# Kernel tuning notes

Hardware: AMD Instinct MI355X
Metric: run time of the kernel (lower is better)

## Reference

```python
import jax, jax.numpy as jnp
import numpy as np

EPS = 1e-12  # torch F.normalize eps
NEG = -9999.0  # masked_fill value from the source


def _l2norm(x):
    n = jnp.linalg.norm(x, axis=-1, keepdims=True)
    return x / jnp.maximum(n, EPS)


def _maxsim(q, d, mask_f, mask_b):
    # q: [B,Lq,D]; d: [N,B,Ld,D]; mask: [N,B,Ld]
    rep = _l2norm(d * mask_f[..., None])
    s = jnp.einsum('bqd,nbkd->nbqk', q, rep)  # [N,B,Lq,Ld]
    s = jnp.where(mask_b[:, :, None, :], s, NEG)
    return s.max(axis=-1).sum(axis=-1)  # [N,B]


def setup_inputs() -> dict:
    key = jax.random.key(0)
    k0, k1, k2, k3, k4 = jax.random.split(key, 5)
    B, N, Lq, Ld, D = 128, 8, 32, 256, 128
    return {
        'q_reps': jax.random.normal(k0, (B, Lq, D), jnp.float32),
        'd_cq': jax.random.normal(k1, (N, B, Ld, D), jnp.float32),
        'd_orig': jax.random.normal(k2, (N, B, Ld, D), jnp.float32),
        'd_mask': jax.random.randint(k3, (N, B, Ld), 0, 2).astype(jnp.int32),
        'labels': jax.random.normal(k4, (B, N), jnp.float32),
    }


def reference(q_reps, d_cq, d_orig, d_mask, labels):
    # teacher='default', loss_type='kldiv' path
    q = _l2norm(q_reps)  # normalize query tokens over D
    mask_f = d_mask.astype(q_reps.dtype)
    mask_b = d_mask.astype(bool)
    scores = _maxsim(q, d_cq, mask_f, mask_b).T        # [B,N] student (cq) MaxSim
    scores_label = _maxsim(q, d_orig, mask_f, mask_b).T  # [B,N] teacher (orig) MaxSim
    # softmax->log in the source == log_softmax (same math, stable form)
    log_s = jax.nn.log_softmax(scores, axis=-1)
    log_t = jax.nn.log_softmax(scores_label, axis=-1)
    # KLDivLoss(reduction='batchmean', log_target=True)
    B = scores.shape[0]
    loss = jnp.sum(jnp.exp(log_t) * (log_t - log_s)) / B
    return loss
```

## Files before the change

### kernel.cpp

```cpp
#include <hip/hip_runtime.h>
#include <math.h>

#define Bq 128
#define Nn 8
#define LQ 32
#define LD 256
#define DD 128
#define EPSN 1e-12f
#define NEGV (-9999.0f)

typedef __attribute__((ext_vector_type(8))) short short8v;
typedef __attribute__((ext_vector_type(4))) int   int4v;
typedef __attribute__((ext_vector_type(4))) float f32x4;

__device__ __forceinline__ unsigned bf16_rne_hibits(float x) {
    unsigned u = __float_as_uint(x);
    return (u + 0x7FFFu + ((u >> 16) & 1u)) & 0xFFFF0000u;
}

__global__ __launch_bounds__(256) void qnorm_k(const float* __restrict__ q,
                                               unsigned short* __restrict__ qh,
                                               unsigned short* __restrict__ ql) {
    int row  = blockIdx.x * 4 + (threadIdx.x >> 6);
    int lane = threadIdx.x & 63;
    size_t base = (size_t)row * DD + lane * 2;
    float2 v = *reinterpret_cast<const float2*>(q + base);
    float ss = v.x * v.x + v.y * v.y;
#pragma unroll
    for (int o = 32; o; o >>= 1) ss += __shfl_xor(ss, o);
    float inv = 1.0f / fmaxf(sqrtf(ss), EPSN);
    float x0 = v.x * inv, x1 = v.y * inv;
    unsigned h0 = bf16_rne_hibits(x0), h1 = bf16_rne_hibits(x1);
    float l0 = x0 - __uint_as_float(h0);
    float l1 = x1 - __uint_as_float(h1);
    unsigned g0 = bf16_rne_hibits(l0), g1 = bf16_rne_hibits(l1);
    unsigned swz = ((unsigned)(lane * 2)) ^ (((unsigned)row & 7u) << 3);
    *reinterpret_cast<unsigned*>(qh + (size_t)row * DD + swz) = (h0 >> 16) | h1;
    *reinterpret_cast<unsigned*>(ql + (size_t)row * DD + swz) = (g0 >> 16) | g1;
}

__global__ __launch_bounds__(256) void maxsim_k(const float* __restrict__ d_cq,
                                                const float* __restrict__ d_orig,
                                                const int* __restrict__ mask,
                                                const unsigned short* __restrict__ qh,
                                                const unsigned short* __restrict__ ql,
                                                float* __restrict__ scores) {
    __shared__ float4 qstage[1024];
    __shared__ float wma[4][32];
    __shared__ float wmb[4][32];

    int nb = blockIdx.x;
    int b  = nb & 127;
    int n  = nb >> 7;

    int tid  = threadIdx.x;
    int w    = tid >> 6;
    int lane = tid & 63;
    int r    = lane & 15;
    int g    = lane >> 4;

    {
        const float4* srch = reinterpret_cast<const float4*>(qh + (size_t)b * LQ * DD);
        const float4* srcl = reinterpret_cast<const float4*>(ql + (size_t)b * LQ * DD);
        qstage[tid]       = srch[tid];
        qstage[tid + 256] = srch[tid + 256];
        qstage[tid + 512] = srcl[tid];
        qstage[tid + 768] = srcl[tid + 256];
    }
    __syncthreads();

    const unsigned short* qh_lds = reinterpret_cast<const unsigned short*>(qstage);
    const unsigned short* ql_lds = qh_lds + LQ * DD;
    unsigned swz8 = ((unsigned)r & 7u) << 3;

    f32x4 rm0a = {NEGV, NEGV, NEGV, NEGV}, rm1a = {NEGV, NEGV, NEGV, NEGV};
    f32x4 rm0b = {NEGV, NEGV, NEGV, NEGV}, rm1b = {NEGV, NEGV, NEGV, NEGV};

#define SB __builtin_amdgcn_sched_barrier(0)

#define CVT2(DH, DL, W, X0, X1, SSQ)                                           \
    { unsigned u0 = __float_as_uint(X0), u1 = __float_as_uint(X1);             \
      DH[W] = (int)((u0 >> 16) | (u1 & 0xFFFF0000u));                          \
      float l0 = (X0) - __uint_as_float(u0 & 0xFFFF0000u);                     \
      float l1 = (X1) - __uint_as_float(u1 & 0xFFFF0000u);                     \
      DL[W] = (int)((__float_as_uint(l0) >> 16) |                              \
                    (__float_as_uint(l1) & 0xFFFF0000u));                      \
      SSQ += (X0)*(X0) + (X1)*(X1); }

#define KSTEP(CA0, CA1, CB0, CB1, KS, PFOFF)                                   \
    {                                                                          \
        unsigned aoff = (((unsigned)(KS) * 32u) + (unsigned)g * 8u) ^ swz8;    \
        short8v a0h = *reinterpret_cast<const short8v*>(qh_lds + r * DD + aoff);          \
        short8v a0l = *reinterpret_cast<const short8v*>(ql_lds + r * DD + aoff);          \
        short8v a1h = *reinterpret_cast<const short8v*>(qh_lds + (r + 16) * DD + aoff);   \
        short8v a1l = *reinterpret_cast<const short8v*>(ql_lds + (r + 16) * DD + aoff);   \
        int4v dhwa, dlwa, dhwb, dlwb;                                          \
        CVT2(dhwa, dlwa, 0, CA0.x, CA0.y, ssqa)                                \
        CVT2(dhwa, dlwa, 1, CA0.z, CA0.w, ssqa)                                \
        CVT2(dhwa, dlwa, 2, CA1.x, CA1.y, ssqa)                                \
        CVT2(dhwa, dlwa, 3, CA1.z, CA1.w, ssqa)                                \
        CA0 = *reinterpret_cast<const float4*>(prow_a + (PFOFF));              \
        CA1 = *reinterpret_cast<const float4*>(prow_a + (PFOFF) + 4);          \
        CVT2(dhwb, dlwb, 0, CB0.x, CB0.y, ssqb)                                \
        CVT2(dhwb, dlwb, 1, CB0.z, CB0.w, ssqb)                                \
        CVT2(dhwb, dlwb, 2, CB1.x, CB1.y, ssqb)                                \
        CVT2(dhwb, dlwb, 3, CB1.z, CB1.w, ssqb)                                \
        CB0 = *reinterpret_cast<const float4*>(prow_b + (PFOFF));              \
        CB1 = *reinterpret_cast<const float4*>(prow_b + (PFOFF) + 4);          \
        short8v dha = __builtin_bit_cast(short8v, dhwa);                       \
        short8v dla = __builtin_bit_cast(short8v, dlwa);                       \
        c0a = __builtin_amdgcn_mfma_f32_16x16x32_bf16(a0h, dha, c0a, 0, 0, 0); \
        c1a = __builtin_amdgcn_mfma_f32_16x16x32_bf16(a1h, dha, c1a, 0, 0, 0); \
        c0a = __builtin_amdgcn_mfma_f32_16x16x32_bf16(a0h, dla, c0a, 0, 0, 0); \
        c1a = __builtin_amdgcn_mfma_f32_16x16x32_bf16(a1h, dla, c1a, 0, 0, 0); \
        c0a = __builtin_amdgcn_mfma_f32_16x16x32_bf16(a0l, dha, c0a, 0, 0, 0); \
        c1a = __builtin_amdgcn_mfma_f32_16x16x32_bf16(a1l, dha, c1a, 0, 0, 0); \
        short8v dhb = __builtin_bit_cast(short8v, dhwb);                       \
        short8v dlb = __builtin_bit_cast(short8v, dlwb);                       \
        c0b = __builtin_amdgcn_mfma_f32_16x16x32_bf16(a0h, dhb, c0b, 0, 0, 0); \
        c1b = __builtin_amdgcn_mfma_f32_16x16x32_bf16(a1h, dhb, c1b, 0, 0, 0); \
        c0b = __builtin_amdgcn_mfma_f32_16x16x32_bf16(a0h, dlb, c0b, 0, 0, 0); \
        c1b = __builtin_amdgcn_mfma_f32_16x16x32_bf16(a1h, dlb, c1b, 0, 0, 0); \
        c0b = __builtin_amdgcn_mfma_f32_16x16x32_bf16(a0l, dhb, c0b, 0, 0, 0); \
        c1b = __builtin_amdgcn_mfma_f32_16x16x32_bf16(a1l, dhb, c1b, 0, 0, 0); \
    }

    const float* prow_a = d_cq   + (size_t)nb * (LD * DD) + (size_t)(w * 64 + r) * DD + g * 8;
    const float* prow_b = d_orig + (size_t)nb * (LD * DD) + (size_t)(w * 64 + r) * DD + g * 8;

    float4 Xa0 = *reinterpret_cast<const float4*>(prow_a);
    float4 Xa1 = *reinterpret_cast<const float4*>(prow_a + 4);
    float4 Xb0 = *reinterpret_cast<const float4*>(prow_b);
    float4 Xb1 = *reinterpret_cast<const float4*>(prow_b + 4);
    float4 Ya0 = *reinterpret_cast<const float4*>(prow_a + 32);
    float4 Ya1 = *reinterpret_cast<const float4*>(prow_a + 36);
    float4 Yb0 = *reinterpret_cast<const float4*>(prow_b + 32);
    float4 Yb1 = *reinterpret_cast<const float4*>(prow_b + 36);

#pragma unroll 1
    for (int nt = 0; nt < 4; ++nt) {
        int drow = w * 64 + nt * 16 + r;

        f32x4 c0a = {0.f, 0.f, 0.f, 0.f}, c1a = {0.f, 0.f, 0.f, 0.f};
        f32x4 c0b = {0.f, 0.f, 0.f, 0.f}, c1b = {0.f, 0.f, 0.f, 0.f};
        float ssqa = 0.0f, ssqb = 0.0f;

        int mk = mask[(size_t)nb * LD + drow];
        int nnoff = (nt < 3) ? 2048 : 0;

        KSTEP(Xa0, Xa1, Xb0, Xb1, 0, 64);         SB;
        KSTEP(Ya0, Ya1, Yb0, Yb1, 1, 96);         SB;
        KSTEP(Xa0, Xa1, Xb0, Xb1, 2, nnoff);      SB;
        KSTEP(Ya0, Ya1, Yb0, Yb1, 3, nnoff + 32); SB;

        ssqa += __shfl_xor(ssqa, 16);  ssqa += __shfl_xor(ssqa, 32);
        ssqb += __shfl_xor(ssqb, 16);  ssqb += __shfl_xor(ssqb, 32);
        float inva = 1.0f / fmaxf(sqrtf(ssqa), EPSN);
        float invb = 1.0f / fmaxf(sqrtf(ssqb), EPSN);

#pragma unroll
        for (int i = 0; i < 4; ++i) {
            rm0a[i] = fmaxf(rm0a[i], mk ? c0a[i] * inva : NEGV);
            rm1a[i] = fmaxf(rm1a[i], mk ? c1a[i] * inva : NEGV);
            rm0b[i] = fmaxf(rm0b[i], mk ? c0b[i] * invb : NEGV);
            rm1b[i] = fmaxf(rm1b[i], mk ? c1b[i] * invb : NEGV);
        }
        prow_a += 16 * DD;
        prow_b += 16 * DD;
    }
#undef KSTEP
#undef CVT2

#pragma unroll
    for (int i = 0; i < 4; ++i) {
#pragma unroll
        for (int o = 1; o <= 8; o <<= 1) {
            rm0a[i] = fmaxf(rm0a[i], __shfl_xor(rm0a[i], o));
            rm1a[i] = fmaxf(rm1a[i], __shfl_xor(rm1a[i], o));
            rm0b[i] = fmaxf(rm0b[i], __shfl_xor(rm0b[i], o));
            rm1b[i] = fmaxf(rm1b[i], __shfl_xor(rm1b[i], o));
        }
    }
    if (r == 0) {
#pragma unroll
        for (int i = 0; i < 4; ++i) {
            wma[w][g * 4 + i]      = rm0a[i];
            wma[w][16 + g * 4 + i] = rm1a[i];
            wmb[w][g * 4 + i]      = rm0b[i];
            wmb[w][16 + g * 4 + i] = rm1b[i];
        }
    }
    __syncthreads();

    if (tid < 64) {
        int tau = tid >> 5, l = tid & 31;
        const float (*wm)[32] = tau ? wmb : wma;
        float v = fmaxf(fmaxf(wm[0][l], wm[1][l]),
                        fmaxf(wm[2][l], wm[3][l]));
#pragma unroll
        for (int o = 1; o <= 16; o <<= 1) v += __shfl_xor(v, o);
        if (l == 0)
            scores[tau * (Bq * Nn) + b * Nn + n] = v;
    }
}

__global__ void loss_k(const float* __restrict__ scores, float* __restrict__ out) {
    int tid = threadIdx.x;
    const float* s = scores + tid * Nn;
    const float* t = scores + Bq * Nn + tid * Nn;
    float sv[Nn], tv[Nn];
#pragma unroll
    for (int n = 0; n < Nn; ++n) { sv[n] = s[n]; tv[n] = t[n]; }
    float ms = sv[0], mt = tv[0];
#pragma unroll
    for (int n = 1; n < Nn; ++n) { ms = fmaxf(ms, sv[n]); mt = fmaxf(mt, tv[n]); }
    float es = 0.0f, et = 0.0f;
#pragma unroll
    for (int n = 0; n < Nn; ++n) { es += expf(sv[n] - ms); et += expf(tv[n] - mt); }
    float lses = ms + logf(es);
    float lset = mt + logf(et);
    double kl = 0.0;
#pragma unroll
    for (int n = 0; n < Nn; ++n) {
        float lt = tv[n] - lset;
        float ls = sv[n] - lses;
        kl += (double)expf(lt) * ((double)lt - (double)ls);
    }
#pragma unroll
    for (int o = 32; o; o >>= 1) kl += __shfl_xor(kl, o);
    __shared__ double part[2];
    if ((tid & 63) == 0) part[tid >> 6] = kl;
    __syncthreads();
    if (tid == 0) out[0] = (float)((part[0] + part[1]) / (double)Bq);
}

extern "C" void kernel_launch(void* const* d_in, const int* in_sizes, int n_in,
                              void* d_out, int out_size, void* d_ws, size_t ws_size,
                              hipStream_t stream) {
    const float* q     = (const float*)d_in[0];
    const float* dcq   = (const float*)d_in[1];
    const float* dorig = (const float*)d_in[2];
    const int*   mask  = (const int*)d_in[3];

    unsigned short* qh = (unsigned short*)d_ws;
    unsigned short* ql = qh + (size_t)Bq * LQ * DD;
    float* scores      = (float*)(ql + (size_t)Bq * LQ * DD);

    qnorm_k<<<(Bq * LQ) / 4, 256, 0, stream>>>(q, qh, ql);
    maxsim_k<<<Nn * Bq, 256, 0, stream>>>(dcq, dorig, mask, qh, ql, scores);
    loss_k<<<1, 128, 0, stream>>>(scores, (float*)d_out);
}
```

Measured before the change: 63.46 us.

## Deepen register prefetch to a full next row tile and cap occupancy

The d_cq/d_orig loads are restructured so each k-chunk's registers (P,Q,R,S) are refilled with the same chunk of the next 16-row tile, instead of two X/Y buffers that were reloaded mid-tile. This makes the prefetch distance one full row tile, giving global loads more time to arrive before the MFMAs use them. The launch bound now requests 4 blocks per SM to cap register use. The doubled prefetch registers raise VGPR pressure and could cause spills or lower occupancy.

```diff
diff --git a/kernel.cpp b/kernel.cpp
--- a/kernel.cpp
+++ b/kernel.cpp
@@ -39,12 +39,12 @@
     *reinterpret_cast<unsigned*>(ql + (size_t)row * DD + swz) = (g0 >> 16) | g1;
 }
 
-__global__ __launch_bounds__(256) void maxsim_k(const float* __restrict__ d_cq,
-                                                const float* __restrict__ d_orig,
-                                                const int* __restrict__ mask,
-                                                const unsigned short* __restrict__ qh,
-                                                const unsigned short* __restrict__ ql,
-                                                float* __restrict__ scores) {
+__global__ __launch_bounds__(256, 4) void maxsim_k(const float* __restrict__ d_cq,
+                                                   const float* __restrict__ d_orig,
+                                                   const int* __restrict__ mask,
+                                                   const unsigned short* __restrict__ qh,
+                                                   const unsigned short* __restrict__ ql,
+                                                   float* __restrict__ scores) {
     __shared__ float4 qstage[1024];
     __shared__ float wma[4][32];
     __shared__ float wmb[4][32];
@@ -128,14 +128,22 @@
     const float* prow_a = d_cq   + (size_t)nb * (LD * DD) + (size_t)(w * 64 + r) * DD + g * 8;
     const float* prow_b = d_orig + (size_t)nb * (LD * DD) + (size_t)(w * 64 + r) * DD + g * 8;
 
-    float4 Xa0 = *reinterpret_cast<const float4*>(prow_a);
-    float4 Xa1 = *reinterpret_cast<const float4*>(prow_a + 4);
-    float4 Xb0 = *reinterpret_cast<const float4*>(prow_b);
-    float4 Xb1 = *reinterpret_cast<const float4*>(prow_b + 4);
-    float4 Ya0 = *reinterpret_cast<const float4*>(prow_a + 32);
-    float4 Ya1 = *reinterpret_cast<const float4*>(prow_a + 36);
-    float4 Yb0 = *reinterpret_cast<const float4*>(prow_b + 32);
-    float4 Yb1 = *reinterpret_cast<const float4*>(prow_b + 36);
+    float4 Pa0 = *reinterpret_cast<const float4*>(prow_a);
+    float4 Pa1 = *reinterpret_cast<const float4*>(prow_a + 4);
+    float4 Pb0 = *reinterpret_cast<const float4*>(prow_b);
+    float4 Pb1 = *reinterpret_cast<const float4*>(prow_b + 4);
+    float4 Qa0 = *reinterpret_cast<const float4*>(prow_a + 32);
+    float4 Qa1 = *reinterpret_cast<const float4*>(prow_a + 36);
+    float4 Qb0 = *reinterpret_cast<const float4*>(prow_b + 32);
+    float4 Qb1 = *reinterpret_cast<const float4*>(prow_b + 36);
+    float4 Ra0 = *reinterpret_cast<const float4*>(prow_a + 64);
+    float4 Ra1 = *reinterpret_cast<const float4*>(prow_a + 68);
+    float4 Rb0 = *reinterpret_cast<const float4*>(prow_b + 64);
+    float4 Rb1 = *reinterpret_cast<const float4*>(prow_b + 68);
+    float4 Sa0 = *reinterpret_cast<const float4*>(prow_a + 96);
+    float4 Sa1 = *reinterpret_cast<const float4*>(prow_a + 100);
+    float4 Sb0 = *reinterpret_cast<const float4*>(prow_b + 96);
+    float4 Sb1 = *reinterpret_cast<const float4*>(prow_b + 100);
 
 #pragma unroll 1
     for (int nt = 0; nt < 4; ++nt) {
@@ -148,10 +156,10 @@
         int mk = mask[(size_t)nb * LD + drow];
         int nnoff = (nt < 3) ? 2048 : 0;
 
-        KSTEP(Xa0, Xa1, Xb0, Xb1, 0, 64);         SB;
-        KSTEP(Ya0, Ya1, Yb0, Yb1, 1, 96);         SB;
-        KSTEP(Xa0, Xa1, Xb0, Xb1, 2, nnoff);      SB;
-        KSTEP(Ya0, Ya1, Yb0, Yb1, 3, nnoff + 32); SB;
+        KSTEP(Pa0, Pa1, Pb0, Pb1, 0, nnoff);      SB;
+        KSTEP(Qa0, Qa1, Qb0, Qb1, 1, nnoff + 32); SB;
+        KSTEP(Ra0, Ra1, Rb0, Rb1, 2, nnoff + 64); SB;
+        KSTEP(Sa0, Sa1, Sb0, Sb1, 3, nnoff + 96); SB;
 
         ssqa += __shfl_xor(ssqa, 16);  ssqa += __shfl_xor(ssqa, 32);
         ssqb += __shfl_xor(ssqb, 16);  ssqb += __shfl_xor(ssqb, 32);
```

New measurement: 117.2 us. 1.85x slower.
